# Optimization experiments

Measured on AMD Instinct MI355X. Metric: run time of the kernel, lower is better.

The kernel has to match this reference:

```python
import jax, jax.numpy as jnp
import numpy as np

N_PROJ, N_SP, D, H = 400000, 40000, 256, 8
DH = D // H  # 32
EPS = 1e-5
NEG_SLOPE = 0.2  # GATv2Conv default


def layer_norm(x, g, b):
    m = x.mean(-1, keepdims=True)
    v = ((x - m) ** 2).mean(-1, keepdims=True)
    return (x - m) / jnp.sqrt(v + EPS) * g + b


def setup_inputs() -> dict:
    key = jax.random.key(0)
    ks = jax.random.split(key, 8)
    w = lambda k, shape: jax.random.normal(k, shape, jnp.float32) * 0.05
    return dict(
        proj_features=jax.random.normal(ks[0], (N_PROJ, D), jnp.float32),
        prev_scenepoint_features=jax.random.normal(ks[1], (N_SP, D), jnp.float32),
        Wl=w(ks[2], (D, D)), bl=jnp.zeros((D,), jnp.float32),
        Wr=w(ks[3], (D, D)), br=jnp.zeros((D,), jnp.float32),
        att=w(ks[4], (H, DH)), gat_bias=jnp.zeros((D,), jnp.float32),
        ln1_g=jnp.ones((D,), jnp.float32), ln1_b=jnp.zeros((D,), jnp.float32),
        ln2_g=jnp.ones((D,), jnp.float32), ln2_b=jnp.zeros((D,), jnp.float32),
        mlp_W=w(ks[5], (D, D)), mlp_b=jnp.zeros((D,), jnp.float32),
        edge_src=jnp.arange(N_PROJ, dtype=jnp.int32),
        edge_tgt=jax.random.randint(ks[6], (N_PROJ,), 0, N_SP, jnp.int32),
    )


def reference(proj_features, prev_scenepoint_features, Wl, bl, Wr, br, att,
              gat_bias, ln1_g, ln1_b, ln2_g, ln2_b, mlp_W, mlp_b,
              edge_src, edge_tgt):
    # norm_and_proj_scenepoint2proj: LayerNorm + ReLU (no Linear: dims equal)
    x_agg = jax.nn.relu(layer_norm(prev_scenepoint_features, ln1_g, ln1_b))

    # GATv2Conv: lin_l on source (projection) nodes, lin_r on target (scene point) nodes
    xl = (proj_features @ Wl + bl).reshape(N_PROJ, H, DH)   # [Np,H,DH]
    xr = (x_agg @ Wr + br).reshape(N_SP, H, DH)             # [Ns,H,DH]
    xl_e = xl[edge_src]                                     # [E,H,DH]
    xr_e = xr[edge_tgt]                                     # [E,H,DH]
    e = jnp.einsum('ehd,hd->eh', jax.nn.leaky_relu(xl_e + xr_e, NEG_SLOPE), att)

    # segment softmax over edges sharing the same target scene point
    e_max = jax.ops.segment_max(e, edge_tgt, num_segments=N_SP)
    ex = jnp.exp(e - e_max[edge_tgt])
    denom = jax.ops.segment_sum(ex, edge_tgt, num_segments=N_SP)
    alpha = ex / (denom[edge_tgt] + 1e-16)                  # [E,H]

    out = jax.ops.segment_sum(alpha[..., None] * xl_e, edge_tgt, num_segments=N_SP)
    x = out.reshape(N_SP, D) + gat_bias                     # concat heads + bias

    # stateful residual with previous scene point features
    x = prev_scenepoint_features + x
    x_skip = x
    # norm_pre_mlp + ReLU, then mlp (single Linear since n_hidden_layers=0)
    x = jax.nn.relu(layer_norm(x, ln2_g, ln2_b))
    x = x @ mlp_W + mlp_b
    return x_skip + x
```

## Files before the change

### kernel.cpp

```cpp
#include <hip/hip_runtime.h>
#include <hip/hip_bf16.h>

#define D_DIM 256
#define H_HEADS 8
#define DH_DIM 32
#define EPS_LN 1e-5f
#define NEG_SLOPE 0.2f

typedef __bf16 bf16x8 __attribute__((ext_vector_type(8)));
typedef unsigned short ushortx8 __attribute__((ext_vector_type(8)));
typedef float floatx4 __attribute__((ext_vector_type(4)));

__device__ inline unsigned short f2bf(float f) {
    __hip_bfloat16 h = __float2bfloat16(f);
    return __builtin_bit_cast(unsigned short, h);
}
__device__ inline float bf2f(unsigned short u) {
    unsigned int x = ((unsigned int)u) << 16;
    return __builtin_bit_cast(float, x);
}

__global__ void wtrans_kernel(const float* __restrict__ W, unsigned short* __restrict__ Wt) {
    int idx = blockIdx.x * 256 + threadIdx.x;
    int n = idx >> 8, k = idx & 255;
    Wt[n * 256 + k] = f2bf(W[k * 256 + n]);
}

__global__ __launch_bounds__(256) void ln_relu_kernel(
        const float* __restrict__ x, const float* __restrict__ g,
        const float* __restrict__ b, float* __restrict__ y, int nrows) {
    int row = blockIdx.x * 4 + (threadIdx.x >> 6);
    if (row >= nrows) return;
    int lane = threadIdx.x & 63;
    const float* xp = x + (size_t)row * D_DIM;
    float v[4], s = 0.f, s2 = 0.f;
#pragma unroll
    for (int j = 0; j < 4; ++j) {
        v[j] = xp[lane + 64 * j];
        s += v[j]; s2 += v[j] * v[j];
    }
#pragma unroll
    for (int m = 32; m >= 1; m >>= 1) {
        s += __shfl_xor(s, m, 64);
        s2 += __shfl_xor(s2, m, 64);
    }
    float mean = s * (1.f / D_DIM);
    float var = s2 * (1.f / D_DIM) - mean * mean;
    float rstd = rsqrtf(var + EPS_LN);
    float* yp = y + (size_t)row * D_DIM;
#pragma unroll
    for (int j = 0; j < 4; ++j) {
        int d = lane + 64 * j;
        float t = (v[j] - mean) * rstd * g[d] + b[d];
        yp[d] = fmaxf(t, 0.f);
    }
}

template <int OUT_BF16, int HAS_RES>
__global__ __launch_bounds__(256) void gemm256_kernel(
        const float* __restrict__ A, const unsigned short* __restrict__ Wt,
        const float* __restrict__ bias, const float* __restrict__ res,
        void* __restrict__ out, int M) {
    __shared__ unsigned short As[128 * 40];
    __shared__ unsigned short Bs[128 * 40];
    const int n0 = blockIdx.x * 128;
    const int m0 = blockIdx.y * 128;
    const int t = threadIdx.x;
    const int lane = t & 63;
    const int wave = t >> 6;
    const int q = lane >> 4;
    const int l16 = lane & 15;
    const int wm = (wave & 1) * 64;
    const int wn = (wave >> 1) * 64;
    const int sm = t >> 1;
    const int sh = t & 1;

    floatx4 acc[4][4] = {};

    for (int kt = 0; kt < 8; ++kt) {
        const int k0 = kt * 32;
        {
            int r = m0 + sm;
            unsigned short tmp[16];
            if (r < M) {
                const float4* ap = (const float4*)(A + (size_t)r * 256 + k0 + sh * 16);
#pragma unroll
                for (int i = 0; i < 4; ++i) {
                    float4 v = ap[i];
                    tmp[i * 4 + 0] = f2bf(v.x);
                    tmp[i * 4 + 1] = f2bf(v.y);
                    tmp[i * 4 + 2] = f2bf(v.z);
                    tmp[i * 4 + 3] = f2bf(v.w);
                }
            } else {
#pragma unroll
                for (int i = 0; i < 16; ++i) tmp[i] = 0;
            }
            *(ushortx8*)&As[sm * 40 + sh * 16] = *(ushortx8*)&tmp[0];
            *(ushortx8*)&As[sm * 40 + sh * 16 + 8] = *(ushortx8*)&tmp[8];
        }
        {
            const unsigned short* wp = Wt + (size_t)(n0 + sm) * 256 + k0 + sh * 16;
            ushortx8 b0 = *(const ushortx8*)wp;
            ushortx8 b1 = *(const ushortx8*)(wp + 8);
            *(ushortx8*)&Bs[sm * 40 + sh * 16] = b0;
            *(ushortx8*)&Bs[sm * 40 + sh * 16 + 8] = b1;
        }
        __syncthreads();
        bf16x8 af[4], bfr[4];
#pragma unroll
        for (int mi = 0; mi < 4; ++mi)
            af[mi] = __builtin_bit_cast(bf16x8,
                *(const ushortx8*)&As[(wm + mi * 16 + l16) * 40 + q * 8]);
#pragma unroll
        for (int ni = 0; ni < 4; ++ni)
            bfr[ni] = __builtin_bit_cast(bf16x8,
                *(const ushortx8*)&Bs[(wn + ni * 16 + l16) * 40 + q * 8]);
#pragma unroll
        for (int mi = 0; mi < 4; ++mi)
#pragma unroll
            for (int ni = 0; ni < 4; ++ni)
                acc[mi][ni] = __builtin_amdgcn_mfma_f32_16x16x32_bf16(
                    af[mi], bfr[ni], acc[mi][ni], 0, 0, 0);
        __syncthreads();
    }
#pragma unroll
    for (int mi = 0; mi < 4; ++mi) {
#pragma unroll
        for (int ni = 0; ni < 4; ++ni) {
            int col = n0 + wn + ni * 16 + l16;
            float bcol = bias[col];
#pragma unroll
            for (int r = 0; r < 4; ++r) {
                int row = m0 + wm + mi * 16 + q * 4 + r;
                if (row < M) {
                    float v = acc[mi][ni][r] + bcol;
                    if (HAS_RES) v += res[(size_t)row * 256 + col];
                    if (OUT_BF16)
                        ((unsigned short*)out)[(size_t)row * 256 + col] = f2bf(v);
                    else
                        ((float*)out)[(size_t)row * 256 + col] = v;
                }
            }
        }
    }
}

__global__ void hist_kernel(const int* __restrict__ tgt, int* __restrict__ counts, int E) {
    int i = blockIdx.x * 256 + threadIdx.x;
    if (i < E) atomicAdd(&counts[tgt[i]], 1);
}

__global__ __launch_bounds__(1024) void scan_kernel(
        const int* __restrict__ counts, int* __restrict__ offs, int n) {
    __shared__ int lds[1024];
    int t = threadIdx.x;
    int CH = (n + 1023) >> 10;
    int beg = t * CH, end = min(beg + CH, n);
    int s = 0;
    for (int i = beg; i < end; ++i) s += counts[i];
    lds[t] = s;
    __syncthreads();
    for (int off = 1; off < 1024; off <<= 1) {
        int v = (t >= off) ? lds[t - off] : 0;
        __syncthreads();
        lds[t] += v;
        __syncthreads();
    }
    int run = lds[t] - s;
    for (int i = beg; i < end; ++i) { offs[i] = run; run += counts[i]; }
    if (t == 1023) offs[n] = lds[1023];
}

__global__ void scatter_kernel(const int* __restrict__ tgt, const int* __restrict__ offs,
                               int* __restrict__ cursor, int* __restrict__ elist, int E) {
    int i = blockIdx.x * 256 + threadIdx.x;
    if (i < E) {
        int tg = tgt[i];
        int p = atomicAdd(&cursor[tg], 1);
        elist[offs[tg] + p] = i;
    }
}

__global__ __launch_bounds__(256) void aggregate_kernel(
        const unsigned short* __restrict__ xl, const float* __restrict__ xr,
        const float* __restrict__ prev, const int* __restrict__ esrc,
        const int* __restrict__ elist, const int* __restrict__ offs,
        const float* __restrict__ att, const float* __restrict__ gbias,
        const float* __restrict__ g2, const float* __restrict__ b2,
        float* __restrict__ x_skip, float* __restrict__ h2, int nsp) {
    int tgt = blockIdx.x * 4 + (threadIdx.x >> 6);
    if (tgt >= nsp) return;
    int lane = threadIdx.x & 63;
    float xrv[4], attv[4], acc[4] = {0.f, 0.f, 0.f, 0.f}, den[4] = {0.f, 0.f, 0.f, 0.f};
#pragma unroll
    for (int j = 0; j < 4; ++j) {
        int d = lane + 64 * j;
        xrv[j] = xr[(size_t)tgt * D_DIM + d];
        attv[j] = att[d];
    }
    int beg = offs[tgt], end = offs[tgt + 1];
    for (int i = beg; i < end; ++i) {
        int e = elist[i];
        int src = esrc[e];
        const unsigned short* xp = xl + (size_t)src * D_DIM;
        float xlv[4], p[4];
#pragma unroll
        for (int j = 0; j < 4; ++j) {
            xlv[j] = bf2f(xp[lane + 64 * j]);
            float tsum = xlv[j] + xrv[j];
            float lr = tsum > 0.f ? tsum : NEG_SLOPE * tsum;
            p[j] = lr * attv[j];
        }
#pragma unroll
        for (int m = 16; m >= 1; m >>= 1) {
#pragma unroll
            for (int j = 0; j < 4; ++j) p[j] += __shfl_xor(p[j], m, 64);
        }
#pragma unroll
        for (int j = 0; j < 4; ++j) {
            float ex = __expf(p[j]);
            den[j] += ex;
            acc[j] += ex * xlv[j];
        }
    }
    float x[4], s = 0.f, s2 = 0.f;
#pragma unroll
    for (int j = 0; j < 4; ++j) {
        int d = lane + 64 * j;
        float o = acc[j] / (den[j] + 1e-16f);
        float v = prev[(size_t)tgt * D_DIM + d] + o + gbias[d];
        x[j] = v; s += v; s2 += v * v;
    }
#pragma unroll
    for (int m = 32; m >= 1; m >>= 1) {
        s += __shfl_xor(s, m, 64);
        s2 += __shfl_xor(s2, m, 64);
    }
    float mean = s * (1.f / D_DIM);
    float var = s2 * (1.f / D_DIM) - mean * mean;
    float rstd = rsqrtf(var + EPS_LN);
#pragma unroll
    for (int j = 0; j < 4; ++j) {
        int d = lane + 64 * j;
        x_skip[(size_t)tgt * D_DIM + d] = x[j];
        float t2 = (x[j] - mean) * rstd * g2[d] + b2[d];
        h2[(size_t)tgt * D_DIM + d] = fmaxf(t2, 0.f);
    }
}

extern "C" void kernel_launch(void* const* d_in, const int* in_sizes, int n_in,
                              void* d_out, int out_size, void* d_ws, size_t ws_size,
                              hipStream_t stream) {
    const float* proj = (const float*)d_in[0];
    const float* prev = (const float*)d_in[1];
    const float* Wl   = (const float*)d_in[2];
    const float* bl   = (const float*)d_in[3];
    const float* Wr   = (const float*)d_in[4];
    const float* br   = (const float*)d_in[5];
    const float* att  = (const float*)d_in[6];
    const float* gbias= (const float*)d_in[7];
    const float* ln1g = (const float*)d_in[8];
    const float* ln1b = (const float*)d_in[9];
    const float* ln2g = (const float*)d_in[10];
    const float* ln2b = (const float*)d_in[11];
    const float* Wm   = (const float*)d_in[12];
    const float* mb   = (const float*)d_in[13];
    const int* esrc   = (const int*)d_in[14];
    const int* etgt   = (const int*)d_in[15];

    const int NP = in_sizes[0] / D_DIM;
    const int NS = in_sizes[1] / D_DIM;
    const int E  = in_sizes[14];

    char* base = (char*)d_ws;
    size_t off = 0;
    auto carve = [&](size_t bytes) {
        char* p = base + off;
        off += (bytes + 255) & ~(size_t)255;
        return p;
    };
    unsigned short* xl    = (unsigned short*)carve((size_t)NP * D_DIM * 2);
    float* x_agg          = (float*)carve((size_t)NS * D_DIM * 4);
    float* xr             = (float*)carve((size_t)NS * D_DIM * 4);
    float* x_skip         = (float*)carve((size_t)NS * D_DIM * 4);
    float* h2             = (float*)carve((size_t)NS * D_DIM * 4);
    unsigned short* Wt_l  = (unsigned short*)carve((size_t)D_DIM * D_DIM * 2);
    unsigned short* Wt_r  = (unsigned short*)carve((size_t)D_DIM * D_DIM * 2);
    unsigned short* Wt_m  = (unsigned short*)carve((size_t)D_DIM * D_DIM * 2);
    int* counts           = (int*)carve((size_t)NS * 4 * 2);
    int* cursor           = counts + NS;
    int* offs             = (int*)carve((size_t)(NS + 1) * 4);
    int* elist            = (int*)carve((size_t)E * 4);

    hipMemsetAsync(counts, 0, (size_t)NS * 4 * 2, stream);

    wtrans_kernel<<<256, 256, 0, stream>>>(Wl, Wt_l);
    wtrans_kernel<<<256, 256, 0, stream>>>(Wr, Wt_r);
    wtrans_kernel<<<256, 256, 0, stream>>>(Wm, Wt_m);

    ln_relu_kernel<<<(NS + 3) / 4, 256, 0, stream>>>(prev, ln1g, ln1b, x_agg, NS);

    gemm256_kernel<0, 0><<<dim3(2, (NS + 127) / 128), 256, 0, stream>>>(
        x_agg, Wt_r, br, nullptr, (void*)xr, NS);

    gemm256_kernel<1, 0><<<dim3(2, (NP + 127) / 128), 256, 0, stream>>>(
        proj, Wt_l, bl, nullptr, (void*)xl, NP);

    hist_kernel<<<(E + 255) / 256, 256, 0, stream>>>(etgt, counts, E);
    scan_kernel<<<1, 1024, 0, stream>>>(counts, offs, NS);
    scatter_kernel<<<(E + 255) / 256, 256, 0, stream>>>(etgt, offs, cursor, elist, E);

    aggregate_kernel<<<(NS + 3) / 4, 256, 0, stream>>>(
        xl, xr, prev, esrc, elist, offs, att, gbias, ln2g, ln2b, x_skip, h2, NS);

    gemm256_kernel<0, 1><<<dim3(2, (NS + 127) / 128), 256, 0, stream>>>(
        h2, Wt_m, mb, x_skip, d_out, NS);
}
```

Before: 1.022 ms.

## Double-buffer GEMM tiles, vectorize aggregate/LN, prefetch edges, fuse weight transposes

The GEMM now uses double-buffered shared-memory tiles, issuing global loads for the next K slice before the MFMAs on the current one, which removes one barrier per iteration. The aggregate kernel switches to a contiguous 4-element-per-lane layout, so each head's dot product reduces over 8 lanes with 3 shuffles. It also prefetches the next edge's source row and computes the softmax denominator once per lane. The LayerNorm kernel and epilogue use float4 loads and stores, and the three weight transposes merge into one LDS-tiled launch. Double buffering doubles LDS use per block and adds register pressure, which could lower occupancy.

Measured after the change: 1.048 ms. +2.5%, slower.

```diff
diff --git a/kernel.cpp b/kernel.cpp
--- a/kernel.cpp
+++ b/kernel.cpp
@@ -2,13 +2,12 @@
 #include <hip/hip_bf16.h>
 
 #define D_DIM 256
-#define H_HEADS 8
-#define DH_DIM 32
 #define EPS_LN 1e-5f
 #define NEG_SLOPE 0.2f
 
 typedef __bf16 bf16x8 __attribute__((ext_vector_type(8)));
 typedef unsigned short ushortx8 __attribute__((ext_vector_type(8)));
+typedef unsigned short ushortx4 __attribute__((ext_vector_type(4)));
 typedef float floatx4 __attribute__((ext_vector_type(4)));
 
 __device__ inline unsigned short f2bf(float f) {
@@ -20,10 +19,29 @@
     return __builtin_bit_cast(float, x);
 }
 
-__global__ void wtrans_kernel(const float* __restrict__ W, unsigned short* __restrict__ Wt) {
-    int idx = blockIdx.x * 256 + threadIdx.x;
-    int n = idx >> 8, k = idx & 255;
-    Wt[n * 256 + k] = f2bf(W[k * 256 + n]);
+__global__ __launch_bounds__(256) void wtrans_kernel(
+        const float* __restrict__ W0, const float* __restrict__ W1,
+        const float* __restrict__ W2, unsigned short* __restrict__ T0,
+        unsigned short* __restrict__ T1, unsigned short* __restrict__ T2) {
+    const float* W = (blockIdx.y == 0) ? W0 : (blockIdx.y == 1) ? W1 : W2;
+    unsigned short* T = (blockIdx.y == 0) ? T0 : (blockIdx.y == 1) ? T1 : T2;
+    __shared__ float lds[64][65];
+    const int tx = blockIdx.x & 3;
+    const int ty = blockIdx.x >> 2;
+    const int t = threadIdx.x;
+    const int r = t >> 6;
+    const int c = t & 63;
+#pragma unroll
+    for (int i = 0; i < 16; ++i) {
+        int row = ty * 64 + r + i * 4;
+        lds[r + i * 4][c] = W[row * 256 + tx * 64 + c];
+    }
+    __syncthreads();
+#pragma unroll
+    for (int i = 0; i < 16; ++i) {
+        int orow = tx * 64 + r + i * 4;
+        T[orow * 256 + ty * 64 + c] = f2bf(lds[c][r + i * 4]);
+    }
 }
 
 __global__ __launch_bounds__(256) void ln_relu_kernel(
@@ -32,13 +50,9 @@
     int row = blockIdx.x * 4 + (threadIdx.x >> 6);
     if (row >= nrows) return;
     int lane = threadIdx.x & 63;
-    const float* xp = x + (size_t)row * D_DIM;
-    float v[4], s = 0.f, s2 = 0.f;
-#pragma unroll
-    for (int j = 0; j < 4; ++j) {
-        v[j] = xp[lane + 64 * j];
-        s += v[j]; s2 += v[j] * v[j];
-    }
+    float4 v = ((const float4*)(x + (size_t)row * D_DIM))[lane];
+    float s = v.x + v.y + v.z + v.w;
+    float s2 = v.x * v.x + v.y * v.y + v.z * v.z + v.w * v.w;
 #pragma unroll
     for (int m = 32; m >= 1; m >>= 1) {
         s += __shfl_xor(s, m, 64);
@@ -47,13 +61,14 @@
     float mean = s * (1.f / D_DIM);
     float var = s2 * (1.f / D_DIM) - mean * mean;
     float rstd = rsqrtf(var + EPS_LN);
-    float* yp = y + (size_t)row * D_DIM;
-#pragma unroll
-    for (int j = 0; j < 4; ++j) {
-        int d = lane + 64 * j;
-        float t = (v[j] - mean) * rstd * g[d] + b[d];
-        yp[d] = fmaxf(t, 0.f);
-    }
+    float4 gv = ((const float4*)g)[lane];
+    float4 bv = ((const float4*)b)[lane];
+    float4 o;
+    o.x = fmaxf((v.x - mean) * rstd * gv.x + bv.x, 0.f);
+    o.y = fmaxf((v.y - mean) * rstd * gv.y + bv.y, 0.f);
+    o.z = fmaxf((v.z - mean) * rstd * gv.z + bv.z, 0.f);
+    o.w = fmaxf((v.w - mean) * rstd * gv.w + bv.w, 0.f);
+    ((float4*)(y + (size_t)row * D_DIM))[lane] = o;
 }
 
 template <int OUT_BF16, int HAS_RES>
@@ -61,8 +76,8 @@
         const float* __restrict__ A, const unsigned short* __restrict__ Wt,
         const float* __restrict__ bias, const float* __restrict__ res,
         void* __restrict__ out, int M) {
-    __shared__ unsigned short As[128 * 40];
-    __shared__ unsigned short Bs[128 * 40];
+    __shared__ unsigned short As[2][128 * 40];
+    __shared__ unsigned short Bs[2][128 * 40];
     const int n0 = blockIdx.x * 128;
     const int m0 = blockIdx.y * 128;
     const int t = threadIdx.x;
@@ -75,55 +90,71 @@
     const int sm = t >> 1;
     const int sh = t & 1;
 
+    const bool arow_ok = (m0 + sm) < M;
+    const float* aptr = A + (size_t)(m0 + sm) * 256 + sh * 16;
+    const unsigned short* bptr = Wt + (size_t)(n0 + sm) * 256 + sh * 16;
+
+    float4 a_reg[4];
+    ushortx8 b_reg[2];
+
+    auto g_load = [&](int kt) {
+        if (arow_ok) {
+            const float4* ap = (const float4*)(aptr + kt * 32);
+            a_reg[0] = ap[0]; a_reg[1] = ap[1]; a_reg[2] = ap[2]; a_reg[3] = ap[3];
+        }
+        const ushortx8* bp = (const ushortx8*)(bptr + kt * 32);
+        b_reg[0] = bp[0]; b_reg[1] = bp[1];
+    };
+    auto s_store = [&](int buf) {
+        unsigned short tmp[16];
+        if (arow_ok) {
+#pragma unroll
+            for (int i = 0; i < 4; ++i) {
+                tmp[i * 4 + 0] = f2bf(a_reg[i].x);
+                tmp[i * 4 + 1] = f2bf(a_reg[i].y);
+                tmp[i * 4 + 2] = f2bf(a_reg[i].z);
+                tmp[i * 4 + 3] = f2bf(a_reg[i].w);
+            }
+        } else {
+#pragma unroll
+            for (int i = 0; i < 16; ++i) tmp[i] = 0;
+        }
+        *(ushortx8*)&As[buf][sm * 40 + sh * 16] = *(ushortx8*)&tmp[0];
+        *(ushortx8*)&As[buf][sm * 40 + sh * 16 + 8] = *(ushortx8*)&tmp[8];
+        *(ushortx8*)&Bs[buf][sm * 40 + sh * 16] = b_reg[0];
+        *(ushortx8*)&Bs[buf][sm * 40 + sh * 16 + 8] = b_reg[1];
+    };
+
     floatx4 acc[4][4] = {};
 
+    g_load(0);
+    s_store(0);
+    __syncthreads();
+
     for (int kt = 0; kt < 8; ++kt) {
-        const int k0 = kt * 32;
-        {
-            int r = m0 + sm;
-            unsigned short tmp[16];
-            if (r < M) {
-                const float4* ap = (const float4*)(A + (size_t)r * 256 + k0 + sh * 16);
-#pragma unroll
-                for (int i = 0; i < 4; ++i) {
-                    float4 v = ap[i];
-                    tmp[i * 4 + 0] = f2bf(v.x);
-                    tmp[i * 4 + 1] = f2bf(v.y);
-                    tmp[i * 4 + 2] = f2bf(v.z);
-                    tmp[i * 4 + 3] = f2bf(v.w);
-                }
-            } else {
-#pragma unroll
-                for (int i = 0; i < 16; ++i) tmp[i] = 0;
-            }
-            *(ushortx8*)&As[sm * 40 + sh * 16] = *(ushortx8*)&tmp[0];
-            *(ushortx8*)&As[sm * 40 + sh * 16 + 8] = *(ushortx8*)&tmp[8];
-        }
-        {
-            const unsigned short* wp = Wt + (size_t)(n0 + sm) * 256 + k0 + sh * 16;
-            ushortx8 b0 = *(const ushortx8*)wp;
-            ushortx8 b1 = *(const ushortx8*)(wp + 8);
-            *(ushortx8*)&Bs[sm * 40 + sh * 16] = b0;
-            *(ushortx8*)&Bs[sm * 40 + sh * 16 + 8] = b1;
-        }
-        __syncthreads();
+        const int cur = kt & 1;
+        if (kt < 7) g_load(kt + 1);
         bf16x8 af[4], bfr[4];
 #pragma unroll
         for (int mi = 0; mi < 4; ++mi)
             af[mi] = __builtin_bit_cast(bf16x8,
-                *(const ushortx8*)&As[(wm + mi * 16 + l16) * 40 + q * 8]);
+                *(const ushortx8*)&As[cur][(wm + mi * 16 + l16) * 40 + q * 8]);
 #pragma unroll
         for (int ni = 0; ni < 4; ++ni)
             bfr[ni] = __builtin_bit_cast(bf16x8,
-                *(const ushortx8*)&Bs[(wn + ni * 16 + l16) * 40 + q * 8]);
+                *(const ushortx8*)&Bs[cur][(wn + ni * 16 + l16) * 40 + q * 8]);
 #pragma unroll
         for (int mi = 0; mi < 4; ++mi)
 #pragma unroll
             for (int ni = 0; ni < 4; ++ni)
                 acc[mi][ni] = __builtin_amdgcn_mfma_f32_16x16x32_bf16(
                     af[mi], bfr[ni], acc[mi][ni], 0, 0, 0);
-        __syncthreads();
-    }
+        if (kt < 7) {
+            s_store(cur ^ 1);
+            __syncthreads();
+        }
+    }
+
 #pragma unroll
     for (int mi = 0; mi < 4; ++mi) {
 #pragma unroll
@@ -192,46 +223,48 @@
     int tgt = blockIdx.x * 4 + (threadIdx.x >> 6);
     if (tgt >= nsp) return;
     int lane = threadIdx.x & 63;
-    float xrv[4], attv[4], acc[4] = {0.f, 0.f, 0.f, 0.f}, den[4] = {0.f, 0.f, 0.f, 0.f};
-#pragma unroll
-    for (int j = 0; j < 4; ++j) {
-        int d = lane + 64 * j;
-        xrv[j] = xr[(size_t)tgt * D_DIM + d];
-        attv[j] = att[d];
-    }
+    float4 xrv = ((const float4*)(xr + (size_t)tgt * D_DIM))[lane];
+    float4 attv = ((const float4*)att)[lane];
+    float acc0 = 0.f, acc1 = 0.f, acc2 = 0.f, acc3 = 0.f, den = 0.f;
     int beg = offs[tgt], end = offs[tgt + 1];
+
+    ushortx4 row = {};
+    if (beg < end) {
+        int e = elist[beg];
+        int src = esrc[e];
+        row = ((const ushortx4*)(xl + (size_t)src * D_DIM))[lane];
+    }
     for (int i = beg; i < end; ++i) {
-        int e = elist[i];
-        int src = esrc[e];
-        const unsigned short* xp = xl + (size_t)src * D_DIM;
-        float xlv[4], p[4];
-#pragma unroll
-        for (int j = 0; j < 4; ++j) {
-            xlv[j] = bf2f(xp[lane + 64 * j]);
-            float tsum = xlv[j] + xrv[j];
-            float lr = tsum > 0.f ? tsum : NEG_SLOPE * tsum;
-            p[j] = lr * attv[j];
-        }
-#pragma unroll
-        for (int m = 16; m >= 1; m >>= 1) {
-#pragma unroll
-            for (int j = 0; j < 4; ++j) p[j] += __shfl_xor(p[j], m, 64);
-        }
-#pragma unroll
-        for (int j = 0; j < 4; ++j) {
-            float ex = __expf(p[j]);
-            den[j] += ex;
-            acc[j] += ex * xlv[j];
-        }
-    }
-    float x[4], s = 0.f, s2 = 0.f;
-#pragma unroll
-    for (int j = 0; j < 4; ++j) {
-        int d = lane + 64 * j;
-        float o = acc[j] / (den[j] + 1e-16f);
-        float v = prev[(size_t)tgt * D_DIM + d] + o + gbias[d];
-        x[j] = v; s += v; s2 += v * v;
-    }
+        ushortx4 row_n = {};
+        if (i + 1 < end) {
+            int e1 = elist[i + 1];
+            int s1 = esrc[e1];
+            row_n = ((const ushortx4*)(xl + (size_t)s1 * D_DIM))[lane];
+        }
+        float x0 = bf2f(row[0]), x1 = bf2f(row[1]), x2 = bf2f(row[2]), x3 = bf2f(row[3]);
+        float t0 = x0 + xrv.x, t1 = x1 + xrv.y, t2 = x2 + xrv.z, t3 = x3 + xrv.w;
+        t0 = t0 > 0.f ? t0 : NEG_SLOPE * t0;
+        t1 = t1 > 0.f ? t1 : NEG_SLOPE * t1;
+        t2 = t2 > 0.f ? t2 : NEG_SLOPE * t2;
+        t3 = t3 > 0.f ? t3 : NEG_SLOPE * t3;
+        float p = t0 * attv.x + t1 * attv.y + t2 * attv.z + t3 * attv.w;
+        p += __shfl_xor(p, 1, 64);
+        p += __shfl_xor(p, 2, 64);
+        p += __shfl_xor(p, 4, 64);
+        float ex = __expf(p);
+        den += ex;
+        acc0 += ex * x0; acc1 += ex * x1; acc2 += ex * x2; acc3 += ex * x3;
+        row = row_n;
+    }
+    float rden = 1.f / (den + 1e-16f);
+    float4 pv = ((const float4*)(prev + (size_t)tgt * D_DIM))[lane];
+    float4 gb = ((const float4*)gbias)[lane];
+    float v0 = pv.x + acc0 * rden + gb.x;
+    float v1 = pv.y + acc1 * rden + gb.y;
+    float v2 = pv.z + acc2 * rden + gb.z;
+    float v3 = pv.w + acc3 * rden + gb.w;
+    float s = v0 + v1 + v2 + v3;
+    float s2 = v0 * v0 + v1 * v1 + v2 * v2 + v3 * v3;
 #pragma unroll
     for (int m = 32; m >= 1; m >>= 1) {
         s += __shfl_xor(s, m, 64);
@@ -240,13 +273,16 @@
     float mean = s * (1.f / D_DIM);
     float var = s2 * (1.f / D_DIM) - mean * mean;
     float rstd = rsqrtf(var + EPS_LN);
-#pragma unroll
-    for (int j = 0; j < 4; ++j) {
-        int d = lane + 64 * j;
-        x_skip[(size_t)tgt * D_DIM + d] = x[j];
-        float t2 = (x[j] - mean) * rstd * g2[d] + b2[d];
-        h2[(size_t)tgt * D_DIM + d] = fmaxf(t2, 0.f);
-    }
+    float4 g2v = ((const float4*)g2)[lane];
+    float4 b2v = ((const float4*)b2)[lane];
+    float4 xs; xs.x = v0; xs.y = v1; xs.z = v2; xs.w = v3;
+    ((float4*)(x_skip + (size_t)tgt * D_DIM))[lane] = xs;
+    float4 h;
+    h.x = fmaxf((v0 - mean) * rstd * g2v.x + b2v.x, 0.f);
+    h.y = fmaxf((v1 - mean) * rstd * g2v.y + b2v.y, 0.f);
+    h.z = fmaxf((v2 - mean) * rstd * g2v.z + b2v.z, 0.f);
+    h.w = fmaxf((v3 - mean) * rstd * g2v.w + b2v.w, 0.f);
+    ((float4*)(h2 + (size_t)tgt * D_DIM))[lane] = h;
 }
 
 extern "C" void kernel_launch(void* const* d_in, const int* in_sizes, int n_in,
@@ -295,9 +331,7 @@
 
     hipMemsetAsync(counts, 0, (size_t)NS * 4 * 2, stream);
 
-    wtrans_kernel<<<256, 256, 0, stream>>>(Wl, Wt_l);
-    wtrans_kernel<<<256, 256, 0, stream>>>(Wr, Wt_r);
-    wtrans_kernel<<<256, 256, 0, stream>>>(Wm, Wt_m);
+    wtrans_kernel<<<dim3(16, 3), 256, 0, stream>>>(Wl, Wr, Wm, Wt_l, Wt_r, Wt_m);
 
     ln_relu_kernel<<<(NS + 3) / 4, 256, 0, stream>>>(prev, ln1g, ln1b, x_agg, NS);
 
```
